# Kernel optimization log

Measured on AMD Instinct MI355X. Metric: run time of the kernel, lower is better.

Reference implementation:

```python
import jax, jax.numpy as jnp
import numpy as np

HEAD_DIM = 64
WIN = 64
SHIFT = WIN // 2  # shift_windows=True
SCALE = HEAD_DIM ** -0.5

_coords = np.arange(WIN)
REL_IDX = (_coords[:, None] - _coords[None, :]) + (WIN - 1)


def _shift_mask(W: int) -> np.ndarray:
    """Swin-style additive shift mask, shape (num_windows, WIN, WIN)."""
    img = np.zeros((W,), dtype=np.float32)
    cnt = 0
    for s in (slice(0, -WIN), slice(-WIN, -SHIFT), slice(-SHIFT, None)):
        img[s] = cnt
        cnt += 1
    mw = img.reshape(W // WIN, WIN)
    diff = mw[:, None, :] - mw[:, :, None]
    return np.where(diff != 0, np.float32(-100.0), np.float32(0.0))


def setup_inputs() -> dict:
    key = jax.random.key(0)
    kq, kk, kv, kb = jax.random.split(key, 4)
    B, W, C = 64, 8192, HEAD_DIM
    q = jax.random.normal(kq, (B, W, C), dtype=jnp.float32)
    k = jax.random.normal(kk, (B, W, C), dtype=jnp.float32)
    v = jax.random.normal(kv, (B, W, C), dtype=jnp.float32)
    rel_bias_table = 0.02 * jax.random.normal(kb, (2 * WIN - 1, 1), dtype=jnp.float32)
    return {"q": q, "k": k, "v": v, "rel_bias_table": rel_bias_table}


def reference(q, k, v, rel_bias_table):
    B, W, C = q.shape
    nw = W // WIN
    mask = jnp.asarray(_shift_mask(W))

    # cyclic shift
    q = jnp.roll(q, -SHIFT, axis=1)
    k = jnp.roll(k, -SHIFT, axis=1)
    v = jnp.roll(v, -SHIFT, axis=1)

    qw = q.reshape(B, nw, WIN, C)
    kw = k.reshape(B, nw, WIN, C)
    vw = v.reshape(B, nw, WIN, C)

    attn = jnp.einsum('bnic,bnjc->bnij', qw, kw) * SCALE
    bias = rel_bias_table[REL_IDX, 0]
    attn = attn + bias[None, None] + mask[None]
    attn = jax.nn.softmax(attn, axis=-1)

    x = jnp.einsum('bnij,bnjc->bnic', attn, vw)
    x = x.reshape(B, W, C)
    x = jnp.roll(x, SHIFT, axis=1)  # reverse cyclic shift
    return x, attn.reshape(-1, WIN, WIN)
```

## Files before the change

### kernel.cpp

```cpp
#include <hip/hip_runtime.h>
#include <hip/hip_bf16.h>

typedef __attribute__((ext_vector_type(8))) short short8;
typedef __attribute__((ext_vector_type(4))) float f32x4;

#define LDST 72
#define MFMA16(a, b, c) __builtin_amdgcn_mfma_f32_16x16x32_bf16(a, b, c, 0, 0, 0)

__device__ __forceinline__ float bf2f(unsigned short h) {
  return __uint_as_float(((unsigned)h) << 16);
}

__global__ __launch_bounds__(256, 4)
void swin64_attn(const float* __restrict__ qg, const float* __restrict__ kg,
                 const float* __restrict__ vg, const float* __restrict__ tbl,
                 float* __restrict__ ox, float* __restrict__ oa) {
  __shared__ unsigned short Khi[64 * LDST], Klo[64 * LDST];
  __shared__ unsigned short Vhi[64 * LDST];
  __shared__ unsigned short Pb[64 * LDST];
  __shared__ float btab[128];

  const int t = threadIdx.x;
  const int b = blockIdx.x >> 7;
  const int n = blockIdx.x & 127;
  const int l = t & 63;
  const int w = t >> 6;
  const int r15 = l & 15;
  const int g4 = l >> 4;
  const int m0 = w * 16;

  const int qrow = (n * 64 + 32 + m0 + r15) & 8191;
  const float* qp = qg + ((size_t)b * 8192 + (size_t)qrow) * 64;
  const float4 qa0 = *(const float4*)(qp + g4 * 8);
  const float4 qa1 = *(const float4*)(qp + g4 * 8 + 4);
  const float4 qa2 = *(const float4*)(qp + 32 + g4 * 8);
  const float4 qa3 = *(const float4*)(qp + 32 + g4 * 8 + 4);

  if (t < 127) btab[t] = tbl[t];

#pragma unroll
  for (int s = 0; s < 2; ++s) {
    const int seg = t + s * 256;
    const int row = seg >> 3;
    const int c8 = seg & 7;
    const int p = (n * 64 + 32 + row) & 8191;
    const size_t g = ((size_t)b * 8192 + (size_t)p) * 64 + (size_t)(c8 * 8);

    {
      const float4 a0 = *(const float4*)(kg + g);
      const float4 a1 = *(const float4*)(kg + g + 4);
      const float f[8] = {a0.x, a0.y, a0.z, a0.w, a1.x, a1.y, a1.z, a1.w};
      unsigned uh[4], ul[4];
#pragma unroll
      for (int i = 0; i < 4; ++i) {
        const unsigned u0 = __float_as_uint(f[2 * i]);
        const unsigned u1 = __float_as_uint(f[2 * i + 1]);
        const float r0 = f[2 * i]     - __uint_as_float(u0 & 0xFFFF0000u);
        const float r1 = f[2 * i + 1] - __uint_as_float(u1 & 0xFFFF0000u);
        uh[i] = (u0 >> 16) | (u1 & 0xFFFF0000u);
        ul[i] = (__float_as_uint(r0) >> 16) | (__float_as_uint(r1) & 0xFFFF0000u);
      }
      *(uint4*)&Khi[row * LDST + c8 * 8] = make_uint4(uh[0], uh[1], uh[2], uh[3]);
      *(uint4*)&Klo[row * LDST + c8 * 8] = make_uint4(ul[0], ul[1], ul[2], ul[3]);
    }
    {
      const float4 a0 = *(const float4*)(vg + g);
      const float4 a1 = *(const float4*)(vg + g + 4);
      const float f[8] = {a0.x, a0.y, a0.z, a0.w, a1.x, a1.y, a1.z, a1.w};
#pragma unroll
      for (int i = 0; i < 8; ++i) {
        const int c = c8 * 8 + i;
        const int idx = c * LDST + ((((row >> 3) ^ ((c >> 3) & 7)) << 3) | (row & 7));
        Vhi[idx] = (unsigned short)((__float_as_uint(f[i]) + 0x8000u) >> 16);
      }
    }
  }

  short8 qh0, qh1, ql0, ql1;
  {
    const float f0[8] = {qa0.x, qa0.y, qa0.z, qa0.w, qa1.x, qa1.y, qa1.z, qa1.w};
    const float f1[8] = {qa2.x, qa2.y, qa2.z, qa2.w, qa3.x, qa3.y, qa3.z, qa3.w};
#pragma unroll
    for (int i = 0; i < 8; ++i) {
      const unsigned u0 = __float_as_uint(f0[i]);
      qh0[i] = (short)(u0 >> 16);
      ql0[i] = (short)(__float_as_uint(f0[i] - __uint_as_float(u0 & 0xFFFF0000u)) >> 16);
      const unsigned u1 = __float_as_uint(f1[i]);
      qh1[i] = (short)(u1 >> 16);
      ql1[i] = (short)(__float_as_uint(f1[i] - __uint_as_float(u1 & 0xFFFF0000u)) >> 16);
    }
  }
  __syncthreads();

  auto ldf = [&](const unsigned short* a, int rb, int kb) -> short8 {
    return *(const short8*)&a[(rb + r15) * LDST + kb * 32 + g4 * 8];
  };
  auto ldv = [&](const unsigned short* a, int rb, int kb) -> short8 {
    const int c = rb + r15;
    const int blk = (kb * 4 + g4) ^ ((c >> 3) & 7);
    return *(const short8*)&a[c * LDST + blk * 8];
  };

  f32x4 acc[4];
#pragma unroll
  for (int nt = 0; nt < 4; ++nt) {
    const short8 kh0 = ldf(Khi, nt * 16, 0), kh1 = ldf(Khi, nt * 16, 1);
    const short8 kl0 = ldf(Klo, nt * 16, 0), kl1 = ldf(Klo, nt * 16, 1);
    f32x4 a = {0.f, 0.f, 0.f, 0.f};
    a = MFMA16(qh0, kh0, a);
    a = MFMA16(qh1, kh1, a);
    a = MFMA16(ql0, kh0, a);
    a = MFMA16(ql1, kh1, a);
    a = MFMA16(qh0, kl0, a);
    a = MFMA16(qh1, kl1, a);
    acc[nt] = a;
  }

  float sv[4][4];
#pragma unroll
  for (int nt = 0; nt < 4; ++nt) {
#pragma unroll
    for (int r = 0; r < 4; ++r) {
      const int i = m0 + g4 * 4 + r;
      const int j = nt * 16 + r15;
      float sx = acc[nt][r] * 0.125f + btab[i - j + 63];
      if (n == 127 && ((i < 32) != (j < 32))) sx -= 100.f;
      sv[nt][r] = sx;
    }
  }

  float mx[4], rinv[4], pr[4][4];
#pragma unroll
  for (int r = 0; r < 4; ++r) {
    float m2 = fmaxf(fmaxf(sv[0][r], sv[1][r]), fmaxf(sv[2][r], sv[3][r]));
    m2 = fmaxf(m2, __shfl_xor(m2, 1));
    m2 = fmaxf(m2, __shfl_xor(m2, 2));
    m2 = fmaxf(m2, __shfl_xor(m2, 4));
    m2 = fmaxf(m2, __shfl_xor(m2, 8));
    mx[r] = m2;
  }
#pragma unroll
  for (int nt = 0; nt < 4; ++nt) {
#pragma unroll
    for (int r = 0; r < 4; ++r) pr[nt][r] = __expf(sv[nt][r] - mx[r]);
  }
#pragma unroll
  for (int r = 0; r < 4; ++r) {
    float s2 = pr[0][r] + pr[1][r] + pr[2][r] + pr[3][r];
    s2 += __shfl_xor(s2, 1);
    s2 += __shfl_xor(s2, 2);
    s2 += __shfl_xor(s2, 4);
    s2 += __shfl_xor(s2, 8);
    rinv[r] = 1.f / s2;
  }

  float* ap = oa + (size_t)blockIdx.x * 4096;
#pragma unroll
  for (int nt = 0; nt < 4; ++nt) {
#pragma unroll
    for (int r = 0; r < 4; ++r) {
      const int i = m0 + g4 * 4 + r;
      const int j = nt * 16 + r15;
      Pb[i * LDST + j] = (unsigned short)((__float_as_uint(pr[nt][r]) + 0x8000u) >> 16);
      ap[i * 64 + j] = pr[nt][r] * rinv[r];
    }
  }
  __syncthreads();

  const short8 pa0 = ldf(Pb, m0, 0), pa1 = ldf(Pb, m0, 1);
#pragma unroll
  for (int ct = 0; ct < 4; ++ct) {
    const short8 vh0 = ldv(Vhi, ct * 16, 0), vh1 = ldv(Vhi, ct * 16, 1);
    f32x4 a = {0.f, 0.f, 0.f, 0.f};
    a = MFMA16(pa0, vh0, a);
    a = MFMA16(pa1, vh1, a);
#pragma unroll
    for (int r = 0; r < 4; ++r) {
      const int i = m0 + g4 * 4 + r;
      const int p2 = (n * 64 + 32 + i) & 8191;
      ox[((size_t)b * 8192 + (size_t)p2) * 64 + ct * 16 + r15] = a[r] * rinv[r];
    }
  }
}

extern "C" void kernel_launch(void* const* d_in, const int* in_sizes, int n_in,
                              void* d_out, int out_size, void* d_ws, size_t ws_size,
                              hipStream_t stream) {
  const float* q = (const float*)d_in[0];
  const float* k = (const float*)d_in[1];
  const float* v = (const float*)d_in[2];
  const float* tbl = (const float*)d_in[3];
  float* ox = (float*)d_out;
  float* oa = ox + (size_t)64 * 8192 * 64;
  swin64_attn<<<dim3(8192), dim3(256), 0, stream>>>(q, k, v, tbl, ox, oa);
}
```

Measured before the change: 125.7 us.

## Process four windows per block with register-prefetched K/V/Q and vectorized attn stores

Each block now loops over four consecutive windows instead of one, prefetching the next window's K, V and Q into registers while computing the current one. The attention-probability output is written through LDS as coalesced float4 stores, reconstructed from the bf16 P buffer, instead of scattered scalar stores. This aims to hide global load latency and improve write coalescing. In exchange it uses fewer blocks, holds more registers for the prefetch, and the stored attn values now carry bf16 rounding, which may hurt accuracy.

```diff
diff --git a/kernel.cpp b/kernel.cpp
--- a/kernel.cpp
+++ b/kernel.cpp
@@ -5,11 +5,10 @@
 typedef __attribute__((ext_vector_type(4))) float f32x4;
 
 #define LDST 72
+#define NW 4
 #define MFMA16(a, b, c) __builtin_amdgcn_mfma_f32_16x16x32_bf16(a, b, c, 0, 0, 0)
 
-__device__ __forceinline__ float bf2f(unsigned short h) {
-  return __uint_as_float(((unsigned)h) << 16);
-}
+#define BARLDS() asm volatile("s_waitcnt lgkmcnt(0)\n\ts_barrier" ::: "memory")
 
 __global__ __launch_bounds__(256, 4)
 void swin64_attn(const float* __restrict__ qg, const float* __restrict__ kg,
@@ -18,79 +17,74 @@
   __shared__ unsigned short Khi[64 * LDST], Klo[64 * LDST];
   __shared__ unsigned short Vhi[64 * LDST];
   __shared__ unsigned short Pb[64 * LDST];
+  __shared__ float rs[64];
   __shared__ float btab[128];
 
   const int t = threadIdx.x;
-  const int b = blockIdx.x >> 7;
-  const int n = blockIdx.x & 127;
+  const int b = blockIdx.x >> 5;
+  const int g = blockIdx.x & 31;
   const int l = t & 63;
   const int w = t >> 6;
   const int r15 = l & 15;
   const int g4 = l >> 4;
   const int m0 = w * 16;
-
-  const int qrow = (n * 64 + 32 + m0 + r15) & 8191;
-  const float* qp = qg + ((size_t)b * 8192 + (size_t)qrow) * 64;
-  const float4 qa0 = *(const float4*)(qp + g4 * 8);
-  const float4 qa1 = *(const float4*)(qp + g4 * 8 + 4);
-  const float4 qa2 = *(const float4*)(qp + 32 + g4 * 8);
-  const float4 qa3 = *(const float4*)(qp + 32 + g4 * 8 + 4);
+  const int row0 = t >> 3;
+  const int c8 = t & 7;
+  const size_t bbase = (size_t)b * 8192;
 
   if (t < 127) btab[t] = tbl[t];
 
-#pragma unroll
-  for (int s = 0; s < 2; ++s) {
-    const int seg = t + s * 256;
-    const int row = seg >> 3;
-    const int c8 = seg & 7;
-    const int p = (n * 64 + 32 + row) & 8191;
-    const size_t g = ((size_t)b * 8192 + (size_t)p) * 64 + (size_t)(c8 * 8);
-
-    {
-      const float4 a0 = *(const float4*)(kg + g);
-      const float4 a1 = *(const float4*)(kg + g + 4);
-      const float f[8] = {a0.x, a0.y, a0.z, a0.w, a1.x, a1.y, a1.z, a1.w};
-      unsigned uh[4], ul[4];
-#pragma unroll
-      for (int i = 0; i < 4; ++i) {
-        const unsigned u0 = __float_as_uint(f[2 * i]);
-        const unsigned u1 = __float_as_uint(f[2 * i + 1]);
-        const float r0 = f[2 * i]     - __uint_as_float(u0 & 0xFFFF0000u);
-        const float r1 = f[2 * i + 1] - __uint_as_float(u1 & 0xFFFF0000u);
-        uh[i] = (u0 >> 16) | (u1 & 0xFFFF0000u);
-        ul[i] = (__float_as_uint(r0) >> 16) | (__float_as_uint(r1) & 0xFFFF0000u);
-      }
-      *(uint4*)&Khi[row * LDST + c8 * 8] = make_uint4(uh[0], uh[1], uh[2], uh[3]);
-      *(uint4*)&Klo[row * LDST + c8 * 8] = make_uint4(ul[0], ul[1], ul[2], ul[3]);
-    }
-    {
-      const float4 a0 = *(const float4*)(vg + g);
-      const float4 a1 = *(const float4*)(vg + g + 4);
-      const float f[8] = {a0.x, a0.y, a0.z, a0.w, a1.x, a1.y, a1.z, a1.w};
-#pragma unroll
-      for (int i = 0; i < 8; ++i) {
-        const int c = c8 * 8 + i;
-        const int idx = c * LDST + ((((row >> 3) ^ ((c >> 3) & 7)) << 3) | (row & 7));
-        Vhi[idx] = (unsigned short)((__float_as_uint(f[i]) + 0x8000u) >> 16);
-      }
-    }
-  }
-
-  short8 qh0, qh1, ql0, ql1;
-  {
-    const float f0[8] = {qa0.x, qa0.y, qa0.z, qa0.w, qa1.x, qa1.y, qa1.z, qa1.w};
-    const float f1[8] = {qa2.x, qa2.y, qa2.z, qa2.w, qa3.x, qa3.y, qa3.z, qa3.w};
+  float4 pk0, pk1, pk2, pk3, pv0, pv1, pv2, pv3, pq0, pq1, pq2, pq3;
+
+  auto issueKV = [&](int n) {
+    const int p0 = (n * 64 + 32 + row0) & 8191;
+    const int p1 = (n * 64 + 64 + row0) & 8191;
+    const float* k0 = kg + (bbase + p0) * 64 + c8 * 8;
+    const float* k1 = kg + (bbase + p1) * 64 + c8 * 8;
+    const float* v0 = vg + (bbase + p0) * 64 + c8 * 8;
+    const float* v1 = vg + (bbase + p1) * 64 + c8 * 8;
+    pk0 = *(const float4*)k0; pk1 = *(const float4*)(k0 + 4);
+    pk2 = *(const float4*)k1; pk3 = *(const float4*)(k1 + 4);
+    pv0 = *(const float4*)v0; pv1 = *(const float4*)(v0 + 4);
+    pv2 = *(const float4*)v1; pv3 = *(const float4*)(v1 + 4);
+  };
+  auto issueQ = [&](int n) {
+    const int qrow = (n * 64 + 32 + m0 + r15) & 8191;
+    const float* qp = qg + (bbase + qrow) * 64 + g4 * 8;
+    pq0 = *(const float4*)qp;        pq1 = *(const float4*)(qp + 4);
+    pq2 = *(const float4*)(qp + 32); pq3 = *(const float4*)(qp + 36);
+  };
+
+  auto packK = [&](int row, const float4 A, const float4 B) {
+    const float f[8] = {A.x, A.y, A.z, A.w, B.x, B.y, B.z, B.w};
+    unsigned uh[4], ul[4];
+#pragma unroll
+    for (int i = 0; i < 4; ++i) {
+      const unsigned u0 = __float_as_uint(f[2 * i]);
+      const unsigned u1 = __float_as_uint(f[2 * i + 1]);
+      const float r0 = f[2 * i]     - __uint_as_float(u0 & 0xFFFF0000u);
+      const float r1 = f[2 * i + 1] - __uint_as_float(u1 & 0xFFFF0000u);
+      uh[i] = (u0 >> 16) | (u1 & 0xFFFF0000u);
+      ul[i] = (__float_as_uint(r0) >> 16) | (__float_as_uint(r1) & 0xFFFF0000u);
+    }
+    *(uint4*)&Khi[row * LDST + c8 * 8] = make_uint4(uh[0], uh[1], uh[2], uh[3]);
+    *(uint4*)&Klo[row * LDST + c8 * 8] = make_uint4(ul[0], ul[1], ul[2], ul[3]);
+  };
+  auto packV = [&](int row, const float4 A, const float4 B) {
+    const float f[8] = {A.x, A.y, A.z, A.w, B.x, B.y, B.z, B.w};
 #pragma unroll
     for (int i = 0; i < 8; ++i) {
-      const unsigned u0 = __float_as_uint(f0[i]);
-      qh0[i] = (short)(u0 >> 16);
-      ql0[i] = (short)(__float_as_uint(f0[i] - __uint_as_float(u0 & 0xFFFF0000u)) >> 16);
-      const unsigned u1 = __float_as_uint(f1[i]);
-      qh1[i] = (short)(u1 >> 16);
-      ql1[i] = (short)(__float_as_uint(f1[i] - __uint_as_float(u1 & 0xFFFF0000u)) >> 16);
-    }
-  }
-  __syncthreads();
+      const int c = c8 * 8 + i;
+      const int idx = c * LDST + ((((row >> 3) ^ ((c >> 3) & 7)) << 3) | (row & 7));
+      Vhi[idx] = (unsigned short)((__float_as_uint(f[i]) + 0x8000u) >> 16);
+    }
+  };
+  auto stageWrite = [&]() {
+    packK(row0, pk0, pk1);
+    packK(row0 + 32, pk2, pk3);
+    packV(row0, pv0, pv1);
+    packV(row0 + 32, pv2, pv3);
+  };
 
   auto ldf = [&](const unsigned short* a, int rb, int kb) -> short8 {
     return *(const short8*)&a[(rb + r15) * LDST + kb * 32 + g4 * 8];
@@ -101,84 +95,147 @@
     return *(const short8*)&a[c * LDST + blk * 8];
   };
 
-  f32x4 acc[4];
-#pragma unroll
-  for (int nt = 0; nt < 4; ++nt) {
-    const short8 kh0 = ldf(Khi, nt * 16, 0), kh1 = ldf(Khi, nt * 16, 1);
-    const short8 kl0 = ldf(Klo, nt * 16, 0), kl1 = ldf(Klo, nt * 16, 1);
-    f32x4 a = {0.f, 0.f, 0.f, 0.f};
-    a = MFMA16(qh0, kh0, a);
-    a = MFMA16(qh1, kh1, a);
-    a = MFMA16(ql0, kh0, a);
-    a = MFMA16(ql1, kh1, a);
-    a = MFMA16(qh0, kl0, a);
-    a = MFMA16(qh1, kl1, a);
-    acc[nt] = a;
-  }
-
-  float sv[4][4];
-#pragma unroll
-  for (int nt = 0; nt < 4; ++nt) {
+  issueKV(g * NW);
+  issueQ(g * NW);
+  stageWrite();
+  BARLDS();
+
+  for (int j = 0; j < NW; ++j) {
+    const int n = g * NW + j;
+
+    short8 qh0, qh1, ql0, ql1;
+    {
+      const float f0[8] = {pq0.x, pq0.y, pq0.z, pq0.w, pq1.x, pq1.y, pq1.z, pq1.w};
+      const float f1[8] = {pq2.x, pq2.y, pq2.z, pq2.w, pq3.x, pq3.y, pq3.z, pq3.w};
+#pragma unroll
+      for (int i = 0; i < 8; ++i) {
+        const unsigned u0 = __float_as_uint(f0[i]);
+        qh0[i] = (short)(u0 >> 16);
+        ql0[i] = (short)(__float_as_uint(f0[i] - __uint_as_float(u0 & 0xFFFF0000u)) >> 16);
+        const unsigned u1 = __float_as_uint(f1[i]);
+        qh1[i] = (short)(u1 >> 16);
+        ql1[i] = (short)(__float_as_uint(f1[i] - __uint_as_float(u1 & 0xFFFF0000u)) >> 16);
+      }
+    }
+
+    if (j + 1 < NW) { issueKV(n + 1); issueQ(n + 1); }
+
+    f32x4 acc[4];
+#pragma unroll
+    for (int nt = 0; nt < 4; ++nt) {
+      const short8 kh0 = ldf(Khi, nt * 16, 0), kh1 = ldf(Khi, nt * 16, 1);
+      const short8 kl0 = ldf(Klo, nt * 16, 0), kl1 = ldf(Klo, nt * 16, 1);
+      f32x4 a = {0.f, 0.f, 0.f, 0.f};
+      a = MFMA16(qh0, kh0, a);
+      a = MFMA16(qh1, kh1, a);
+      a = MFMA16(ql0, kh0, a);
+      a = MFMA16(ql1, kh1, a);
+      a = MFMA16(qh0, kl0, a);
+      a = MFMA16(qh1, kl1, a);
+      acc[nt] = a;
+    }
+
+#pragma unroll
+    for (int nt = 0; nt < 4; ++nt) {
+#pragma unroll
+      for (int r = 0; r < 4; ++r) {
+        const int i = m0 + g4 * 4 + r;
+        const int jj = nt * 16 + r15;
+        float sx = acc[nt][r] * 0.125f + btab[i - jj + 63];
+        if (n == 127 && ((i < 32) != (jj < 32))) sx -= 100.f;
+        acc[nt][r] = sx;
+      }
+    }
+
+    float mx[4], rinv[4];
 #pragma unroll
     for (int r = 0; r < 4; ++r) {
-      const int i = m0 + g4 * 4 + r;
-      const int j = nt * 16 + r15;
-      float sx = acc[nt][r] * 0.125f + btab[i - j + 63];
-      if (n == 127 && ((i < 32) != (j < 32))) sx -= 100.f;
-      sv[nt][r] = sx;
-    }
-  }
-
-  float mx[4], rinv[4], pr[4][4];
-#pragma unroll
-  for (int r = 0; r < 4; ++r) {
-    float m2 = fmaxf(fmaxf(sv[0][r], sv[1][r]), fmaxf(sv[2][r], sv[3][r]));
-    m2 = fmaxf(m2, __shfl_xor(m2, 1));
-    m2 = fmaxf(m2, __shfl_xor(m2, 2));
-    m2 = fmaxf(m2, __shfl_xor(m2, 4));
-    m2 = fmaxf(m2, __shfl_xor(m2, 8));
-    mx[r] = m2;
-  }
-#pragma unroll
-  for (int nt = 0; nt < 4; ++nt) {
-#pragma unroll
-    for (int r = 0; r < 4; ++r) pr[nt][r] = __expf(sv[nt][r] - mx[r]);
-  }
-#pragma unroll
-  for (int r = 0; r < 4; ++r) {
-    float s2 = pr[0][r] + pr[1][r] + pr[2][r] + pr[3][r];
-    s2 += __shfl_xor(s2, 1);
-    s2 += __shfl_xor(s2, 2);
-    s2 += __shfl_xor(s2, 4);
-    s2 += __shfl_xor(s2, 8);
-    rinv[r] = 1.f / s2;
-  }
-
-  float* ap = oa + (size_t)blockIdx.x * 4096;
-#pragma unroll
-  for (int nt = 0; nt < 4; ++nt) {
+      float m2 = fmaxf(fmaxf(acc[0][r], acc[1][r]), fmaxf(acc[2][r], acc[3][r]));
+      m2 = fmaxf(m2, __shfl_xor(m2, 1));
+      m2 = fmaxf(m2, __shfl_xor(m2, 2));
+      m2 = fmaxf(m2, __shfl_xor(m2, 4));
+      m2 = fmaxf(m2, __shfl_xor(m2, 8));
+      mx[r] = m2;
+    }
+#pragma unroll
+    for (int nt = 0; nt < 4; ++nt) {
+#pragma unroll
+      for (int r = 0; r < 4; ++r) acc[nt][r] = __expf(acc[nt][r] - mx[r]);
+    }
 #pragma unroll
     for (int r = 0; r < 4; ++r) {
-      const int i = m0 + g4 * 4 + r;
-      const int j = nt * 16 + r15;
-      Pb[i * LDST + j] = (unsigned short)((__float_as_uint(pr[nt][r]) + 0x8000u) >> 16);
-      ap[i * 64 + j] = pr[nt][r] * rinv[r];
-    }
-  }
-  __syncthreads();
-
-  const short8 pa0 = ldf(Pb, m0, 0), pa1 = ldf(Pb, m0, 1);
-#pragma unroll
-  for (int ct = 0; ct < 4; ++ct) {
-    const short8 vh0 = ldv(Vhi, ct * 16, 0), vh1 = ldv(Vhi, ct * 16, 1);
-    f32x4 a = {0.f, 0.f, 0.f, 0.f};
-    a = MFMA16(pa0, vh0, a);
-    a = MFMA16(pa1, vh1, a);
-#pragma unroll
-    for (int r = 0; r < 4; ++r) {
-      const int i = m0 + g4 * 4 + r;
-      const int p2 = (n * 64 + 32 + i) & 8191;
-      ox[((size_t)b * 8192 + (size_t)p2) * 64 + ct * 16 + r15] = a[r] * rinv[r];
+      float s2 = acc[0][r] + acc[1][r] + acc[2][r] + acc[3][r];
+      s2 += __shfl_xor(s2, 1);
+      s2 += __shfl_xor(s2, 2);
+      s2 += __shfl_xor(s2, 4);
+      s2 += __shfl_xor(s2, 8);
+      rinv[r] = 1.f / s2;
+    }
+
+#pragma unroll
+    for (int nt = 0; nt < 4; ++nt) {
+#pragma unroll
+      for (int r = 0; r < 4; ++r) {
+        const int i = m0 + g4 * 4 + r;
+        const int jj = nt * 16 + r15;
+        Pb[i * LDST + jj] =
+            (unsigned short)((__float_as_uint(acc[nt][r]) + 0x8000u) >> 16);
+      }
+    }
+    if (r15 == 0) {
+#pragma unroll
+      for (int r = 0; r < 4; ++r) rs[m0 + g4 * 4 + r] = rinv[r];
+    }
+    BARLDS();
+
+    const short8 pa0 = ldf(Pb, m0, 0), pa1 = ldf(Pb, m0, 1);
+#pragma unroll
+    for (int ct = 0; ct < 4; ++ct) {
+      const short8 vh0 = ldv(Vhi, ct * 16, 0), vh1 = ldv(Vhi, ct * 16, 1);
+      f32x4 a = {0.f, 0.f, 0.f, 0.f};
+      a = MFMA16(pa0, vh0, a);
+      a = MFMA16(pa1, vh1, a);
+#pragma unroll
+      for (int r = 0; r < 4; ++r) {
+        const int i = m0 + g4 * 4 + r;
+        const int p2 = (n * 64 + 32 + i) & 8191;
+        ox[(bbase + p2) * 64 + ct * 16 + r15] = a[r] * rinv[r];
+      }
+    }
+
+    {
+      const int er = t >> 2, ec = (t & 3) << 4;
+      const float ri = rs[er];
+      const uint4 u0 = *(const uint4*)&Pb[er * LDST + ec];
+      const uint4 u1 = *(const uint4*)&Pb[er * LDST + ec + 8];
+      float* apo = oa + ((size_t)(b * 128 + n)) * 4096 + er * 64 + ec;
+      float4 o;
+      o.x = __uint_as_float(u0.x << 16) * ri;
+      o.y = __uint_as_float(u0.x & 0xFFFF0000u) * ri;
+      o.z = __uint_as_float(u0.y << 16) * ri;
+      o.w = __uint_as_float(u0.y & 0xFFFF0000u) * ri;
+      *(float4*)apo = o;
+      o.x = __uint_as_float(u0.z << 16) * ri;
+      o.y = __uint_as_float(u0.z & 0xFFFF0000u) * ri;
+      o.z = __uint_as_float(u0.w << 16) * ri;
+      o.w = __uint_as_float(u0.w & 0xFFFF0000u) * ri;
+      *(float4*)(apo + 4) = o;
+      o.x = __uint_as_float(u1.x << 16) * ri;
+      o.y = __uint_as_float(u1.x & 0xFFFF0000u) * ri;
+      o.z = __uint_as_float(u1.y << 16) * ri;
+      o.w = __uint_as_float(u1.y & 0xFFFF0000u) * ri;
+      *(float4*)(apo + 8) = o;
+      o.x = __uint_as_float(u1.z << 16) * ri;
+      o.y = __uint_as_float(u1.z & 0xFFFF0000u) * ri;
+      o.z = __uint_as_float(u1.w << 16) * ri;
+      o.w = __uint_as_float(u1.w & 0xFFFF0000u) * ri;
+      *(float4*)(apo + 12) = o;
+    }
+
+    if (j + 1 < NW) {
+      BARLDS();
+      stageWrite();
+      BARLDS();
     }
   }
 }
@@ -192,5 +249,5 @@
   const float* tbl = (const float*)d_in[3];
   float* ox = (float*)d_out;
   float* oa = ox + (size_t)64 * 8192 * 64;
-  swin64_attn<<<dim3(8192), dim3(256), 0, stream>>>(q, k, v, tbl, ox, oa);
+  swin64_attn<<<dim3(64 * 32), dim3(256), 0, stream>>>(q, k, v, tbl, ox, oa);
 }
```

New measurement: 183.0 us. 1.46x slower.

## Load K/V fragments directly from global into registers, drop shared staging

Applied to the files above, without the earlier changes.

Each wave now loads its K and V MFMA operand fragments straight from global memory into registers and converts them to bf16 there, replacing the block-wide shared-memory staging of K and V. The bias table is read directly per element, and the block-wide barriers are replaced with a wave-local LDS wait, since each wave only reads back its own P rows. This removes LDS traffic and __syncthreads, at the cost of each of the four waves re-reading all of K and V from global/L2. V is gathered with scalar strided loads, and launch bounds are relaxed to allow more registers.

```diff
diff --git a/kernel.cpp b/kernel.cpp
--- a/kernel.cpp
+++ b/kernel.cpp
@@ -7,18 +7,11 @@
 #define LDST 72
 #define MFMA16(a, b, c) __builtin_amdgcn_mfma_f32_16x16x32_bf16(a, b, c, 0, 0, 0)
 
-__device__ __forceinline__ float bf2f(unsigned short h) {
-  return __uint_as_float(((unsigned)h) << 16);
-}
-
-__global__ __launch_bounds__(256, 4)
+__global__ __launch_bounds__(256, 2)
 void swin64_attn(const float* __restrict__ qg, const float* __restrict__ kg,
                  const float* __restrict__ vg, const float* __restrict__ tbl,
                  float* __restrict__ ox, float* __restrict__ oa) {
-  __shared__ unsigned short Khi[64 * LDST], Klo[64 * LDST];
-  __shared__ unsigned short Vhi[64 * LDST];
   __shared__ unsigned short Pb[64 * LDST];
-  __shared__ float btab[128];
 
   const int t = threadIdx.x;
   const int b = blockIdx.x >> 7;
@@ -28,53 +21,54 @@
   const int r15 = l & 15;
   const int g4 = l >> 4;
   const int m0 = w * 16;
+  const size_t bbase = (size_t)b * 8192;
+  const int R0 = n * 64 + 32;
 
-  const int qrow = (n * 64 + 32 + m0 + r15) & 8191;
-  const float* qp = qg + ((size_t)b * 8192 + (size_t)qrow) * 64;
-  const float4 qa0 = *(const float4*)(qp + g4 * 8);
-  const float4 qa1 = *(const float4*)(qp + g4 * 8 + 4);
-  const float4 qa2 = *(const float4*)(qp + 32 + g4 * 8);
-  const float4 qa3 = *(const float4*)(qp + 32 + g4 * 8 + 4);
+  const int qrow = (R0 + m0 + r15) & 8191;
+  const float* qp = qg + (bbase + qrow) * 64 + g4 * 8;
+  const float4 qa0 = *(const float4*)qp;
+  const float4 qa1 = *(const float4*)(qp + 4);
+  const float4 qa2 = *(const float4*)(qp + 32);
+  const float4 qa3 = *(const float4*)(qp + 36);
 
-  if (t < 127) btab[t] = tbl[t];
+  float4 kfa[4][2], kfb[4][2];
+#pragma unroll
+  for (int nt = 0; nt < 4; ++nt) {
+    const int krow = (R0 + nt * 16 + r15) & 8191;
+    const float* kp = kg + (bbase + krow) * 64 + g4 * 8;
+#pragma unroll
+    for (int kb = 0; kb < 2; ++kb) {
+      kfa[nt][kb] = *(const float4*)(kp + kb * 32);
+      kfb[nt][kb] = *(const float4*)(kp + kb * 32 + 4);
+    }
+  }
 
+  short8 vfr[4][2];
 #pragma unroll
-  for (int s = 0; s < 2; ++s) {
-    const int seg = t + s * 256;
-    const int row = seg >> 3;
-    const int c8 = seg & 7;
-    const int p = (n * 64 + 32 + row) & 8191;
-    const size_t g = ((size_t)b * 8192 + (size_t)p) * 64 + (size_t)(c8 * 8);
-
-    {
-      const float4 a0 = *(const float4*)(kg + g);
-      const float4 a1 = *(const float4*)(kg + g + 4);
-      const float f[8] = {a0.x, a0.y, a0.z, a0.w, a1.x, a1.y, a1.z, a1.w};
-      unsigned uh[4], ul[4];
+  for (int ct = 0; ct < 4; ++ct) {
 #pragma unroll
-      for (int i = 0; i < 4; ++i) {
-        const unsigned u0 = __float_as_uint(f[2 * i]);
-        const unsigned u1 = __float_as_uint(f[2 * i + 1]);
-        const float r0 = f[2 * i]     - __uint_as_float(u0 & 0xFFFF0000u);
-        const float r1 = f[2 * i + 1] - __uint_as_float(u1 & 0xFFFF0000u);
-        uh[i] = (u0 >> 16) | (u1 & 0xFFFF0000u);
-        ul[i] = (__float_as_uint(r0) >> 16) | (__float_as_uint(r1) & 0xFFFF0000u);
-      }
-      *(uint4*)&Khi[row * LDST + c8 * 8] = make_uint4(uh[0], uh[1], uh[2], uh[3]);
-      *(uint4*)&Klo[row * LDST + c8 * 8] = make_uint4(ul[0], ul[1], ul[2], ul[3]);
-    }
-    {
-      const float4 a0 = *(const float4*)(vg + g);
-      const float4 a1 = *(const float4*)(vg + g + 4);
-      const float f[8] = {a0.x, a0.y, a0.z, a0.w, a1.x, a1.y, a1.z, a1.w};
+    for (int kb = 0; kb < 2; ++kb) {
+      const int c = ct * 16 + r15;
+      float vt[8];
 #pragma unroll
       for (int i = 0; i < 8; ++i) {
-        const int c = c8 * 8 + i;
-        const int idx = c * LDST + ((((row >> 3) ^ ((c >> 3) & 7)) << 3) | (row & 7));
-        Vhi[idx] = (unsigned short)((__float_as_uint(f[i]) + 0x8000u) >> 16);
+        const int p = (R0 + kb * 32 + g4 * 8 + i) & 8191;
+        vt[i] = vg[(bbase + p) * 64 + c];
       }
+      short8 v8;
+#pragma unroll
+      for (int i = 0; i < 8; ++i)
+        v8[i] = (short)(unsigned short)((__float_as_uint(vt[i]) + 0x8000u) >> 16);
+      vfr[ct][kb] = v8;
     }
   }
+
+  float bv[4][4];
+#pragma unroll
+  for (int nt = 0; nt < 4; ++nt)
+#pragma unroll
+    for (int r = 0; r < 4; ++r)
+      bv[nt][r] = tbl[(m0 + g4 * 4 + r) - (nt * 16 + r15) + 63];
 
   short8 qh0, qh1, ql0, ql1;
   {
@@ -90,49 +84,51 @@
       ql1[i] = (short)(__float_as_uint(f1[i] - __uint_as_float(u1 & 0xFFFF0000u)) >> 16);
     }
   }
-  __syncthreads();
-
-  auto ldf = [&](const unsigned short* a, int rb, int kb) -> short8 {
-    return *(const short8*)&a[(rb + r15) * LDST + kb * 32 + g4 * 8];
-  };
-  auto ldv = [&](const unsigned short* a, int rb, int kb) -> short8 {
-    const int c = rb + r15;
-    const int blk = (kb * 4 + g4) ^ ((c >> 3) & 7);
-    return *(const short8*)&a[c * LDST + blk * 8];
-  };
 
   f32x4 acc[4];
 #pragma unroll
   for (int nt = 0; nt < 4; ++nt) {
-    const short8 kh0 = ldf(Khi, nt * 16, 0), kh1 = ldf(Khi, nt * 16, 1);
-    const short8 kl0 = ldf(Klo, nt * 16, 0), kl1 = ldf(Klo, nt * 16, 1);
+    short8 kh[2], kl[2];
+#pragma unroll
+    for (int kb = 0; kb < 2; ++kb) {
+      const float f[8] = {kfa[nt][kb].x, kfa[nt][kb].y, kfa[nt][kb].z, kfa[nt][kb].w,
+                          kfb[nt][kb].x, kfb[nt][kb].y, kfb[nt][kb].z, kfb[nt][kb].w};
+      short8 h8, l8;
+#pragma unroll
+      for (int i = 0; i < 8; ++i) {
+        const unsigned u = __float_as_uint(f[i]);
+        h8[i] = (short)(u >> 16);
+        l8[i] = (short)(__float_as_uint(f[i] - __uint_as_float(u & 0xFFFF0000u)) >> 16);
+      }
+      kh[kb] = h8;
+      kl[kb] = l8;
+    }
     f32x4 a = {0.f, 0.f, 0.f, 0.f};
-    a = MFMA16(qh0, kh0, a);
-    a = MFMA16(qh1, kh1, a);
-    a = MFMA16(ql0, kh0, a);
-    a = MFMA16(ql1, kh1, a);
-    a = MFMA16(qh0, kl0, a);
-    a = MFMA16(qh1, kl1, a);
+    a = MFMA16(qh0, kh[0], a);
+    a = MFMA16(qh1, kh[1], a);
+    a = MFMA16(ql0, kh[0], a);
+    a = MFMA16(ql1, kh[1], a);
+    a = MFMA16(qh0, kl[0], a);
+    a = MFMA16(qh1, kl[1], a);
     acc[nt] = a;
   }
 
-  float sv[4][4];
 #pragma unroll
   for (int nt = 0; nt < 4; ++nt) {
 #pragma unroll
     for (int r = 0; r < 4; ++r) {
       const int i = m0 + g4 * 4 + r;
       const int j = nt * 16 + r15;
-      float sx = acc[nt][r] * 0.125f + btab[i - j + 63];
+      float sx = acc[nt][r] * 0.125f + bv[nt][r];
       if (n == 127 && ((i < 32) != (j < 32))) sx -= 100.f;
-      sv[nt][r] = sx;
+      acc[nt][r] = sx;
     }
   }
 
-  float mx[4], rinv[4], pr[4][4];
+  float mx[4], rinv[4];
 #pragma unroll
   for (int r = 0; r < 4; ++r) {
-    float m2 = fmaxf(fmaxf(sv[0][r], sv[1][r]), fmaxf(sv[2][r], sv[3][r]));
+    float m2 = fmaxf(fmaxf(acc[0][r], acc[1][r]), fmaxf(acc[2][r], acc[3][r]));
     m2 = fmaxf(m2, __shfl_xor(m2, 1));
     m2 = fmaxf(m2, __shfl_xor(m2, 2));
     m2 = fmaxf(m2, __shfl_xor(m2, 4));
@@ -142,11 +138,11 @@
 #pragma unroll
   for (int nt = 0; nt < 4; ++nt) {
 #pragma unroll
-    for (int r = 0; r < 4; ++r) pr[nt][r] = __expf(sv[nt][r] - mx[r]);
+    for (int r = 0; r < 4; ++r) acc[nt][r] = __expf(acc[nt][r] - mx[r]);
   }
 #pragma unroll
   for (int r = 0; r < 4; ++r) {
-    float s2 = pr[0][r] + pr[1][r] + pr[2][r] + pr[3][r];
+    float s2 = acc[0][r] + acc[1][r] + acc[2][r] + acc[3][r];
     s2 += __shfl_xor(s2, 1);
     s2 += __shfl_xor(s2, 2);
     s2 += __shfl_xor(s2, 4);
@@ -161,24 +157,26 @@
     for (int r = 0; r < 4; ++r) {
       const int i = m0 + g4 * 4 + r;
       const int j = nt * 16 + r15;
-      Pb[i * LDST + j] = (unsigned short)((__float_as_uint(pr[nt][r]) + 0x8000u) >> 16);
-      ap[i * 64 + j] = pr[nt][r] * rinv[r];
+      Pb[i * LDST + j] =
+          (unsigned short)((__float_as_uint(acc[nt][r]) + 0x8000u) >> 16);
+      ap[i * 64 + j] = acc[nt][r] * rinv[r];
     }
   }
-  __syncthreads();
+  asm volatile("s_waitcnt lgkmcnt(0)" ::: "memory");
+  __builtin_amdgcn_sched_barrier(0);
 
-  const short8 pa0 = ldf(Pb, m0, 0), pa1 = ldf(Pb, m0, 1);
+  const short8 pa0 = *(const short8*)&Pb[(m0 + r15) * LDST + g4 * 8];
+  const short8 pa1 = *(const short8*)&Pb[(m0 + r15) * LDST + 32 + g4 * 8];
 #pragma unroll
   for (int ct = 0; ct < 4; ++ct) {
-    const short8 vh0 = ldv(Vhi, ct * 16, 0), vh1 = ldv(Vhi, ct * 16, 1);
     f32x4 a = {0.f, 0.f, 0.f, 0.f};
-    a = MFMA16(pa0, vh0, a);
-    a = MFMA16(pa1, vh1, a);
+    a = MFMA16(pa0, vfr[ct][0], a);
+    a = MFMA16(pa1, vfr[ct][1], a);
 #pragma unroll
     for (int r = 0; r < 4; ++r) {
       const int i = m0 + g4 * 4 + r;
-      const int p2 = (n * 64 + 32 + i) & 8191;
-      ox[((size_t)b * 8192 + (size_t)p2) * 64 + ct * 16 + r15] = a[r] * rinv[r];
+      const int p2 = (R0 + i) & 8191;
+      ox[(bbase + p2) * 64 + ct * 16 + r15] = a[r] * rinv[r];
     }
   }
 }
```

After: 155.5 us. 1.24x slower.
